# Performance work log

Hardware: AMD Instinct MI355X
Metric: run time of the kernel (lower is better)

The kernel has to match this reference:

```python
import jax, jax.numpy as jnp
import numpy as np

NUM_EXPERTS = 64
TOP_K = 2
AUX_COEF = 0.001
Z_COEF = 0.001


def setup_inputs() -> dict:
    key = jax.random.key(0)
    k1, k2 = jax.random.split(key)
    hidden_states = jax.random.normal(k1, (16384, 4096), dtype=jnp.float32)
    W_gate = jax.random.normal(k2, (NUM_EXPERTS, 4096), dtype=jnp.float32) * 0.02
    return {"hidden_states": hidden_states, "W_gate": W_gate}


def reference(hidden_states, W_gate):
    # Gate GEMM: [N, H] x [E, H]^T -> [N, E]
    router_logits = jnp.einsum('nh,eh->ne', hidden_states, W_gate)
    router_probs = jax.nn.softmax(router_logits, axis=-1)

    # Top-k selection + renormalization
    expert_weights, expert_indices = jax.lax.top_k(router_probs, TOP_K)
    expert_weights = expert_weights / jnp.sum(expert_weights, axis=-1, keepdims=True)

    # Load-balancing loss: num_experts * sum_i f_i * P_i
    num_tokens = router_probs.shape[0]
    one_hot = jax.nn.one_hot(expert_indices, NUM_EXPERTS, dtype=jnp.float32)  # [N, K, E]
    tokens_per_expert = one_hot.sum(axis=(0, 1))  # [E]
    f = tokens_per_expert / (num_tokens * TOP_K)
    P = router_probs.mean(axis=0)
    lb_loss = NUM_EXPERTS * jnp.sum(f * P)

    # Z-loss: mean of logsumexp(logits)^2
    log_z = jax.nn.logsumexp(router_logits, axis=-1)
    z_loss = jnp.mean(log_z ** 2)

    aux_loss = AUX_COEF * lb_loss + Z_COEF * z_loss
    return expert_weights, expert_indices, aux_loss
```

## Files before the change

kernel.cpp:

```cpp
#include <hip/hip_runtime.h>
#include <hip/hip_bf16.h>

#define NTOK 16384
#define HD   4096
#define NE   64
#define KSPLIT 4
#define KS    (HD / KSPLIT)
#define NSTEP (KS / 32)
#define SL2   68
#define W2OFF 256
#define W2JSTR 131072

typedef __bf16 bf16x8 __attribute__((ext_vector_type(8)));
typedef float  f32x4  __attribute__((ext_vector_type(4)));

__device__ __forceinline__ f32x4 mfma16(bf16x8 a, bf16x8 b, f32x4 c) {
    return __builtin_amdgcn_mfma_f32_16x16x32_bf16(a, b, c, 0, 0, 0);
}

__global__ void prep_kernel(const float* __restrict__ Wg, float* __restrict__ ws) {
    const int idx = blockIdx.x * 256 + threadIdx.x;
    if (blockIdx.x == 0 && threadIdx.x < 129) ws[threadIdx.x] = 0.0f;
    __bf16* W2 = (__bf16*)(ws + W2OFF);
    const float4* src = (const float4*)(Wg + (size_t)idx * 8);
    float4 q0 = src[0], q1 = src[1];
    float xs[8] = {q0.x, q0.y, q0.z, q0.w, q1.x, q1.y, q1.z, q1.w};
    bf16x8 hi, lo;
    #pragma unroll
    for (int e = 0; e < 8; ++e) {
        __bf16 h = (__bf16)xs[e];
        hi[e] = h;
        lo[e] = (__bf16)(xs[e] - (float)h);
    }
    *(bf16x8*)(W2 + (size_t)idx * 16)     = hi;
    *(bf16x8*)(W2 + (size_t)idx * 16 + 8) = lo;
}

__global__ __launch_bounds__(256, 4) void router_kernel(
    const float* __restrict__ hs,
    float* __restrict__ out,
    float* __restrict__ ws)
{
    __shared__ float sRed[4 * 16 * SL2];
    __shared__ float sInv[16];
    __shared__ float sPp[256];
    __shared__ float sCnt[64];
    __shared__ float sZ;

    const int tid  = threadIdx.x;
    const int t0   = blockIdx.x * 16;
    const int wv   = tid >> 6;
    const int lane = tid & 63;
    const int fm   = lane & 15;
    const int fq   = lane >> 4;

    if (tid < 64) sCnt[tid] = 0.0f;
    if (tid == 0) sZ = 0.0f;

    const __bf16* W2 = (const __bf16*)(ws + W2OFF);
    const int k0 = wv * KS;
    const float* aPtr = hs + (size_t)(t0 + fm) * HD + k0 + fq * 8;
    const int bOff = (fm * 512 + (k0 >> 3) + fq) * 16;

    f32x4 acc[4];
    #pragma unroll
    for (int j = 0; j < 4; ++j) acc[j] = (f32x4){0.f, 0.f, 0.f, 0.f};

    float4 a_raw[2][2];
    bf16x8 b_frag[2][4][2];

    a_raw[0][0] = *(const float4*)(aPtr);
    a_raw[0][1] = *(const float4*)(aPtr + 4);
    #pragma unroll
    for (int j = 0; j < 4; ++j) {
        const __bf16* bp = W2 + j * W2JSTR + bOff;
        b_frag[0][j][0] = *(const bf16x8*)(bp);
        b_frag[0][j][1] = *(const bf16x8*)(bp + 8);
    }

    #pragma unroll 2
    for (int it = 0; it < NSTEP; ++it) {
        const int cur = it & 1, nxt = cur ^ 1;
        if (it + 1 < NSTEP) {
            const float* ap = aPtr + (it + 1) * 32;
            a_raw[nxt][0] = *(const float4*)(ap);
            a_raw[nxt][1] = *(const float4*)(ap + 4);
            const __bf16* bp = W2 + bOff + (it + 1) * 64;
            #pragma unroll
            for (int j = 0; j < 4; ++j) {
                b_frag[nxt][j][0] = *(const bf16x8*)(bp + j * W2JSTR);
                b_frag[nxt][j][1] = *(const bf16x8*)(bp + j * W2JSTR + 8);
            }
        }
        float4 q0 = a_raw[cur][0], q1 = a_raw[cur][1];
        float xs[8] = {q0.x, q0.y, q0.z, q0.w, q1.x, q1.y, q1.z, q1.w};
        bf16x8 ahi, alo;
        #pragma unroll
        for (int e = 0; e < 8; ++e) {
            __bf16 h = (__bf16)xs[e];
            ahi[e] = h;
            alo[e] = (__bf16)(xs[e] - (float)h);
        }
        #pragma unroll
        for (int j = 0; j < 4; ++j) {
            acc[j] = mfma16(ahi, b_frag[cur][j][0], acc[j]);
            acc[j] = mfma16(alo, b_frag[cur][j][0], acc[j]);
            acc[j] = mfma16(ahi, b_frag[cur][j][1], acc[j]);
            acc[j] = mfma16(alo, b_frag[cur][j][1], acc[j]);
        }
    }

    {
        float* my = &sRed[wv * 16 * SL2];
        #pragma unroll
        for (int j = 0; j < 4; ++j)
            #pragma unroll
            for (int r = 0; r < 4; ++r)
                my[(fq * 4 + r) * SL2 + (j * 16 + fm)] = acc[j][r];
    }
    __syncthreads();
    for (int s = tid; s < 1024; s += 256) {
        const int t = s >> 6, e = s & 63;
        const int o = t * SL2 + e;
        sRed[o] = sRed[o] + sRed[16 * SL2 + o] + sRed[32 * SL2 + o] + sRed[48 * SL2 + o];
    }
    __syncthreads();

    const int g = tid >> 4;
    const int l = tid & 15;
    float* Lrow = &sRed[g * SL2 + l * 4];
    float lv[4];
    float m = -3.0e38f;
    #pragma unroll
    for (int c = 0; c < 4; ++c) { lv[c] = Lrow[c]; m = fmaxf(m, lv[c]); }
    m = fmaxf(m, __shfl_xor(m, 1, 64));
    m = fmaxf(m, __shfl_xor(m, 2, 64));
    m = fmaxf(m, __shfl_xor(m, 4, 64));
    m = fmaxf(m, __shfl_xor(m, 8, 64));

    float v1 = -3.0e38f, v2 = -3.0e38f; int i1 = 0, i2 = 0;
    float ssum = 0.0f;
    #pragma unroll
    for (int c = 0; c < 4; ++c) {
        const float val = lv[c]; const int idx = l * 4 + c;
        const float ev = __expf(val - m);
        Lrow[c] = ev;
        ssum += ev;
        if (val > v1) { v2 = v1; i2 = i1; v1 = val; i1 = idx; }
        else if (val > v2) { v2 = val; i2 = idx; }
    }
    ssum += __shfl_xor(ssum, 1, 64);
    ssum += __shfl_xor(ssum, 2, 64);
    ssum += __shfl_xor(ssum, 4, 64);
    ssum += __shfl_xor(ssum, 8, 64);

    #pragma unroll
    for (int s = 1; s <= 8; s <<= 1) {
        const float ov1 = __shfl_xor(v1, s, 64);
        const int   oi1 = __shfl_xor(i1, s, 64);
        const float ov2 = __shfl_xor(v2, s, 64);
        const int   oi2 = __shfl_xor(i2, s, 64);
        float n1, n2; int ni1, ni2;
        const bool ofirst = (ov1 > v1) || (ov1 == v1 && oi1 < i1);
        if (ofirst) {
            n1 = ov1; ni1 = oi1;
            const bool osec = (ov2 > v1) || (ov2 == v1 && oi2 < i1);
            n2 = osec ? ov2 : v1; ni2 = osec ? oi2 : i1;
        } else {
            n1 = v1; ni1 = i1;
            const bool asec = (v2 > ov1) || (v2 == ov1 && i2 < oi1);
            n2 = asec ? v2 : ov1; ni2 = asec ? i2 : oi1;
        }
        v1 = n1; i1 = ni1; v2 = n2; i2 = ni2;
    }

    if (l == 0) {
        const float e1 = __expf(v1 - m), e2 = __expf(v2 - m);
        const float winv = 1.0f / (e1 + e2);
        const int token = t0 + g;
        out[2 * token]     = e1 * winv;
        out[2 * token + 1] = e2 * winv;
        out[2 * NTOK + 2 * token]     = (float)i1;
        out[2 * NTOK + 2 * token + 1] = (float)i2;
        const float lse = m + __logf(ssum);
        atomicAdd(&sZ, lse * lse);
        atomicAdd(&sCnt[i1], 1.0f);
        atomicAdd(&sCnt[i2], 1.0f);
        sInv[g] = 1.0f / ssum;
    }
    __syncthreads();

    {
        const int e = tid & 63;
        const int q = tid >> 6;
        float part = 0.0f;
        #pragma unroll
        for (int t = 0; t < 4; ++t) {
            const int tok = q * 4 + t;
            part += sRed[tok * SL2 + e] * sInv[tok];
        }
        sPp[q * 64 + e] = part;
    }
    __syncthreads();
    if (tid < 64) {
        const float ps = sPp[tid] + sPp[64 + tid] + sPp[128 + tid] + sPp[192 + tid];
        atomicAdd(&ws[tid], ps);
        atomicAdd(&ws[64 + tid], sCnt[tid]);
    }
    if (tid == 0) atomicAdd(&ws[128], sZ);
}

__global__ void finalize_kernel(const float* __restrict__ ws, float* __restrict__ out) {
    const int e = threadIdx.x;
    const float P = ws[e] * (1.0f / NTOK);
    const float f = ws[64 + e] * (1.0f / (NTOK * 2));
    float term = f * P;
    #pragma unroll
    for (int s = 32; s >= 1; s >>= 1) term += __shfl_xor(term, s, 64);
    if (e == 0) {
        const float lb = 64.0f * term;
        const float z  = ws[128] * (1.0f / NTOK);
        out[4 * NTOK] = 0.001f * lb + 0.001f * z;
    }
}

extern "C" void kernel_launch(void* const* d_in, const int* in_sizes, int n_in,
                              void* d_out, int out_size, void* d_ws, size_t ws_size,
                              hipStream_t stream) {
    const float* hs = (const float*)d_in[0];
    const float* Wg = (const float*)d_in[1];
    float* out = (float*)d_out;
    float* ws  = (float*)d_ws;

    hipLaunchKernelGGL(prep_kernel, dim3(128), dim3(256), 0, stream, Wg, ws);
    hipLaunchKernelGGL(router_kernel, dim3(NTOK / 16), dim3(256), 0, stream, hs, out, ws);
    hipLaunchKernelGGL(finalize_kernel, dim3(1), dim3(64), 0, stream, ws, out);
}
```

Before: 430.8 us.

## Split router into K-split GEMM with LDS-staged weights and separate epilogue kernel

After: 542.4 us. 25.9% more time.

```diff
diff --git a/kernel.cpp b/kernel.cpp
--- a/kernel.cpp
+++ b/kernel.cpp
@@ -4,12 +4,14 @@
 #define NTOK 16384
 #define HD   4096
 #define NE   64
-#define KSPLIT 4
+#define KSPLIT 16
 #define KS    (HD / KSPLIT)
 #define NSTEP (KS / 32)
 #define SL2   68
-#define W2OFF 256
-#define W2JSTR 131072
+
+#define W2HI_OFF 256
+#define W2LO_OFF (W2HI_OFF + 131072)
+#define PART_OFF (W2LO_OFF + 131072)
 
 typedef __bf16 bf16x8 __attribute__((ext_vector_type(8)));
 typedef float  f32x4  __attribute__((ext_vector_type(4)));
@@ -21,123 +23,151 @@
 __global__ void prep_kernel(const float* __restrict__ Wg, float* __restrict__ ws) {
     const int idx = blockIdx.x * 256 + threadIdx.x;
     if (blockIdx.x == 0 && threadIdx.x < 129) ws[threadIdx.x] = 0.0f;
-    __bf16* W2 = (__bf16*)(ws + W2OFF);
-    const float4* src = (const float4*)(Wg + (size_t)idx * 8);
-    float4 q0 = src[0], q1 = src[1];
+    const int ln = idx & 63;
+    const int j  = (idx >> 6) & 3;
+    const int s  = (idx >> 8) & 7;
+    const int ks = idx >> 11;
+    const int e  = j * 16 + (ln & 15);
+    const int k  = ks * KS + s * 32 + (ln >> 4) * 8;
+    const float* src = Wg + (size_t)e * HD + k;
+    float4 q0 = *(const float4*)src;
+    float4 q1 = *(const float4*)(src + 4);
     float xs[8] = {q0.x, q0.y, q0.z, q0.w, q1.x, q1.y, q1.z, q1.w};
     bf16x8 hi, lo;
     #pragma unroll
-    for (int e = 0; e < 8; ++e) {
-        __bf16 h = (__bf16)xs[e];
-        hi[e] = h;
-        lo[e] = (__bf16)(xs[e] - (float)h);
-    }
-    *(bf16x8*)(W2 + (size_t)idx * 16)     = hi;
-    *(bf16x8*)(W2 + (size_t)idx * 16 + 8) = lo;
-}
-
-__global__ __launch_bounds__(256, 4) void router_kernel(
-    const float* __restrict__ hs,
-    float* __restrict__ out,
-    float* __restrict__ ws)
+    for (int t = 0; t < 8; ++t) {
+        __bf16 h = (__bf16)xs[t];
+        hi[t] = h;
+        lo[t] = (__bf16)(xs[t] - (float)h);
+    }
+    *((bf16x8*)((__bf16*)(ws + W2HI_OFF)) + idx) = hi;
+    *((bf16x8*)((__bf16*)(ws + W2LO_OFF)) + idx) = lo;
+}
+
+__global__ __launch_bounds__(512, 4) void gemm_kernel(
+    const float* __restrict__ hs, float* __restrict__ ws)
 {
-    __shared__ float sRed[4 * 16 * SL2];
+    __shared__ bf16x8 sBhi[2048];
+    __shared__ bf16x8 sBlo[2048];
+
+    const int tid = threadIdx.x;
+    const int ks  = blockIdx.x & 15;
+    const int tb  = blockIdx.x >> 4;
+
+    {
+        const bf16x8* ghi = (const bf16x8*)((const __bf16*)(ws + W2HI_OFF)) + ks * 2048;
+        const bf16x8* glo = (const bf16x8*)((const __bf16*)(ws + W2LO_OFF)) + ks * 2048;
+        #pragma unroll
+        for (int c = 0; c < 4; ++c) {
+            sBhi[c * 512 + tid] = ghi[c * 512 + tid];
+            sBlo[c * 512 + tid] = glo[c * 512 + tid];
+        }
+    }
+    __syncthreads();
+
+    const int wv   = tid >> 6;
+    const int lane = tid & 63;
+    const int fm   = lane & 15;
+    const int fq   = lane >> 4;
+    float* part = ws + PART_OFF + (size_t)ks * (NTOK * 64);
+
+    #pragma unroll 1
+    for (int g = 0; g < 4; ++g) {
+        const int tok0 = tb * 512 + wv * 64 + g * 16;
+        const float* aPtr = hs + (size_t)(tok0 + fm) * HD + ks * KS + fq * 8;
+
+        f32x4 acc[4];
+        #pragma unroll
+        for (int j = 0; j < 4; ++j) acc[j] = (f32x4){0.f, 0.f, 0.f, 0.f};
+
+        float4 aq[2][2];
+        aq[0][0] = *(const float4*)(aPtr);
+        aq[0][1] = *(const float4*)(aPtr + 4);
+        aq[1][0] = *(const float4*)(aPtr + 32);
+        aq[1][1] = *(const float4*)(aPtr + 36);
+        bf16x8 bh[2][4], bl[2][4];
+        #pragma unroll
+        for (int j = 0; j < 4; ++j) {
+            bh[0][j] = sBhi[j * 64 + lane];
+            bl[0][j] = sBlo[j * 64 + lane];
+        }
+
+        #pragma unroll
+        for (int s = 0; s < NSTEP; ++s) {
+            const int cur = s & 1, nxt = cur ^ 1;
+            float4 q0 = aq[cur][0], q1 = aq[cur][1];
+            if (s + 2 < NSTEP) {
+                aq[cur][0] = *(const float4*)(aPtr + (s + 2) * 32);
+                aq[cur][1] = *(const float4*)(aPtr + (s + 2) * 32 + 4);
+            }
+            if (s + 1 < NSTEP) {
+                #pragma unroll
+                for (int j = 0; j < 4; ++j) {
+                    bh[nxt][j] = sBhi[((s + 1) * 4 + j) * 64 + lane];
+                    bl[nxt][j] = sBlo[((s + 1) * 4 + j) * 64 + lane];
+                }
+            }
+            float xs[8] = {q0.x, q0.y, q0.z, q0.w, q1.x, q1.y, q1.z, q1.w};
+            bf16x8 ahi, alo;
+            #pragma unroll
+            for (int t = 0; t < 8; ++t) {
+                __bf16 h = (__bf16)xs[t];
+                ahi[t] = h;
+                alo[t] = (__bf16)(xs[t] - (float)h);
+            }
+            #pragma unroll
+            for (int j = 0; j < 4; ++j) {
+                acc[j] = mfma16(ahi, bh[cur][j], acc[j]);
+                acc[j] = mfma16(alo, bh[cur][j], acc[j]);
+                acc[j] = mfma16(ahi, bl[cur][j], acc[j]);
+                acc[j] = mfma16(alo, bl[cur][j], acc[j]);
+            }
+        }
+
+        #pragma unroll
+        for (int j = 0; j < 4; ++j)
+            #pragma unroll
+            for (int r = 0; r < 4; ++r)
+                part[(size_t)(tok0 + fq * 4 + r) * 64 + j * 16 + fm] = acc[j][r];
+    }
+}
+
+__global__ __launch_bounds__(256) void epilogue_kernel(
+    float* __restrict__ ws, float* __restrict__ out)
+{
+    __shared__ float sRed[16 * SL2];
     __shared__ float sInv[16];
     __shared__ float sPp[256];
     __shared__ float sCnt[64];
     __shared__ float sZ;
 
-    const int tid  = threadIdx.x;
-    const int t0   = blockIdx.x * 16;
-    const int wv   = tid >> 6;
-    const int lane = tid & 63;
-    const int fm   = lane & 15;
-    const int fq   = lane >> 4;
-
+    const int tid = threadIdx.x;
+    const int t0  = blockIdx.x * 16;
     if (tid < 64) sCnt[tid] = 0.0f;
     if (tid == 0) sZ = 0.0f;
 
-    const __bf16* W2 = (const __bf16*)(ws + W2OFF);
-    const int k0 = wv * KS;
-    const float* aPtr = hs + (size_t)(t0 + fm) * HD + k0 + fq * 8;
-    const int bOff = (fm * 512 + (k0 >> 3) + fq) * 16;
-
-    f32x4 acc[4];
-    #pragma unroll
-    for (int j = 0; j < 4; ++j) acc[j] = (f32x4){0.f, 0.f, 0.f, 0.f};
-
-    float4 a_raw[2][2];
-    bf16x8 b_frag[2][4][2];
-
-    a_raw[0][0] = *(const float4*)(aPtr);
-    a_raw[0][1] = *(const float4*)(aPtr + 4);
-    #pragma unroll
-    for (int j = 0; j < 4; ++j) {
-        const __bf16* bp = W2 + j * W2JSTR + bOff;
-        b_frag[0][j][0] = *(const bf16x8*)(bp);
-        b_frag[0][j][1] = *(const bf16x8*)(bp + 8);
-    }
-
-    #pragma unroll 2
-    for (int it = 0; it < NSTEP; ++it) {
-        const int cur = it & 1, nxt = cur ^ 1;
-        if (it + 1 < NSTEP) {
-            const float* ap = aPtr + (it + 1) * 32;
-            a_raw[nxt][0] = *(const float4*)(ap);
-            a_raw[nxt][1] = *(const float4*)(ap + 4);
-            const __bf16* bp = W2 + bOff + (it + 1) * 64;
-            #pragma unroll
-            for (int j = 0; j < 4; ++j) {
-                b_frag[nxt][j][0] = *(const bf16x8*)(bp + j * W2JSTR);
-                b_frag[nxt][j][1] = *(const bf16x8*)(bp + j * W2JSTR + 8);
-            }
-        }
-        float4 q0 = a_raw[cur][0], q1 = a_raw[cur][1];
-        float xs[8] = {q0.x, q0.y, q0.z, q0.w, q1.x, q1.y, q1.z, q1.w};
-        bf16x8 ahi, alo;
-        #pragma unroll
-        for (int e = 0; e < 8; ++e) {
-            __bf16 h = (__bf16)xs[e];
-            ahi[e] = h;
-            alo[e] = (__bf16)(xs[e] - (float)h);
-        }
-        #pragma unroll
-        for (int j = 0; j < 4; ++j) {
-            acc[j] = mfma16(ahi, b_frag[cur][j][0], acc[j]);
-            acc[j] = mfma16(alo, b_frag[cur][j][0], acc[j]);
-            acc[j] = mfma16(ahi, b_frag[cur][j][1], acc[j]);
-            acc[j] = mfma16(alo, b_frag[cur][j][1], acc[j]);
-        }
-    }
-
-    {
-        float* my = &sRed[wv * 16 * SL2];
-        #pragma unroll
-        for (int j = 0; j < 4; ++j)
-            #pragma unroll
-            for (int r = 0; r < 4; ++r)
-                my[(fq * 4 + r) * SL2 + (j * 16 + fm)] = acc[j][r];
-    }
-    __syncthreads();
-    for (int s = tid; s < 1024; s += 256) {
-        const int t = s >> 6, e = s & 63;
-        const int o = t * SL2 + e;
-        sRed[o] = sRed[o] + sRed[16 * SL2 + o] + sRed[32 * SL2 + o] + sRed[48 * SL2 + o];
-    }
-    __syncthreads();
-
     const int g = tid >> 4;
     const int l = tid & 15;
-    float* Lrow = &sRed[g * SL2 + l * 4];
-    float lv[4];
+    const int tok = t0 + g;
+    const float* pbase = ws + PART_OFF + (size_t)tok * 64 + l * 4;
+    float4 sv = {0.f, 0.f, 0.f, 0.f};
+    #pragma unroll
+    for (int k = 0; k < KSPLIT; ++k) {
+        float4 v = *(const float4*)(pbase + (size_t)k * (NTOK * 64));
+        sv.x += v.x; sv.y += v.y; sv.z += v.z; sv.w += v.w;
+    }
+    float lv[4] = {sv.x, sv.y, sv.z, sv.w};
+    __syncthreads();
+
     float m = -3.0e38f;
     #pragma unroll
-    for (int c = 0; c < 4; ++c) { lv[c] = Lrow[c]; m = fmaxf(m, lv[c]); }
+    for (int c = 0; c < 4; ++c) m = fmaxf(m, lv[c]);
     m = fmaxf(m, __shfl_xor(m, 1, 64));
     m = fmaxf(m, __shfl_xor(m, 2, 64));
     m = fmaxf(m, __shfl_xor(m, 4, 64));
     m = fmaxf(m, __shfl_xor(m, 8, 64));
 
+    float* Lrow = &sRed[g * SL2 + l * 4];
     float v1 = -3.0e38f, v2 = -3.0e38f; int i1 = 0, i2 = 0;
     float ssum = 0.0f;
     #pragma unroll
@@ -177,11 +207,10 @@
     if (l == 0) {
         const float e1 = __expf(v1 - m), e2 = __expf(v2 - m);
         const float winv = 1.0f / (e1 + e2);
-        const int token = t0 + g;
-        out[2 * token]     = e1 * winv;
-        out[2 * token + 1] = e2 * winv;
-        out[2 * NTOK + 2 * token]     = (float)i1;
-        out[2 * NTOK + 2 * token + 1] = (float)i2;
+        out[2 * tok]     = e1 * winv;
+        out[2 * tok + 1] = e2 * winv;
+        out[2 * NTOK + 2 * tok]     = (float)i1;
+        out[2 * NTOK + 2 * tok + 1] = (float)i2;
         const float lse = m + __logf(ssum);
         atomicAdd(&sZ, lse * lse);
         atomicAdd(&sCnt[i1], 1.0f);
@@ -193,13 +222,13 @@
     {
         const int e = tid & 63;
         const int q = tid >> 6;
-        float part = 0.0f;
+        float p = 0.0f;
         #pragma unroll
         for (int t = 0; t < 4; ++t) {
-            const int tok = q * 4 + t;
-            part += sRed[tok * SL2 + e] * sInv[tok];
-        }
-        sPp[q * 64 + e] = part;
+            const int tk = q * 4 + t;
+            p += sRed[tk * SL2 + e] * sInv[tk];
+        }
+        sPp[q * 64 + e] = p;
     }
     __syncthreads();
     if (tid < 64) {
@@ -233,6 +262,7 @@
     float* ws  = (float*)d_ws;
 
     hipLaunchKernelGGL(prep_kernel, dim3(128), dim3(256), 0, stream, Wg, ws);
-    hipLaunchKernelGGL(router_kernel, dim3(NTOK / 16), dim3(256), 0, stream, hs, out, ws);
+    hipLaunchKernelGGL(gemm_kernel, dim3(512), dim3(512), 0, stream, hs, ws);
+    hipLaunchKernelGGL(epilogue_kernel, dim3(NTOK / 16), dim3(256), 0, stream, ws, out);
     hipLaunchKernelGGL(finalize_kernel, dim3(1), dim3(64), 0, stream, ws, out);
 }
```

## Repack gate weights into fragment order and deepen load prefetch pipeline

Applied to the files above, without the earlier changes.

Measured after the change: 448.9 us. 4.2% more time.

```diff
diff --git a/kernel.cpp b/kernel.cpp
--- a/kernel.cpp
+++ b/kernel.cpp
@@ -4,12 +4,10 @@
 #define NTOK 16384
 #define HD   4096
 #define NE   64
-#define KSPLIT 4
-#define KS    (HD / KSPLIT)
-#define NSTEP (KS / 32)
-#define SL2   68
-#define W2OFF 256
-#define W2JSTR 131072
+#define SL2  68
+
+#define W2HI_OFF 256
+#define W2LO_OFF (W2HI_OFF + 131072)
 
 typedef __bf16 bf16x8 __attribute__((ext_vector_type(8)));
 typedef float  f32x4  __attribute__((ext_vector_type(4)));
@@ -21,22 +19,28 @@
 __global__ void prep_kernel(const float* __restrict__ Wg, float* __restrict__ ws) {
     const int idx = blockIdx.x * 256 + threadIdx.x;
     if (blockIdx.x == 0 && threadIdx.x < 129) ws[threadIdx.x] = 0.0f;
-    __bf16* W2 = (__bf16*)(ws + W2OFF);
-    const float4* src = (const float4*)(Wg + (size_t)idx * 8);
-    float4 q0 = src[0], q1 = src[1];
+    const int ln = idx & 63;
+    const int j  = (idx >> 6) & 3;
+    const int s  = (idx >> 8) & 7;
+    const int ks = idx >> 11;
+    const int e  = j * 16 + (ln & 15);
+    const int k  = ks * 256 + s * 32 + (ln >> 4) * 8;
+    const float* src = Wg + (size_t)e * HD + k;
+    float4 q0 = *(const float4*)src;
+    float4 q1 = *(const float4*)(src + 4);
     float xs[8] = {q0.x, q0.y, q0.z, q0.w, q1.x, q1.y, q1.z, q1.w};
     bf16x8 hi, lo;
     #pragma unroll
-    for (int e = 0; e < 8; ++e) {
-        __bf16 h = (__bf16)xs[e];
-        hi[e] = h;
-        lo[e] = (__bf16)(xs[e] - (float)h);
-    }
-    *(bf16x8*)(W2 + (size_t)idx * 16)     = hi;
-    *(bf16x8*)(W2 + (size_t)idx * 16 + 8) = lo;
-}
-
-__global__ __launch_bounds__(256, 4) void router_kernel(
+    for (int t = 0; t < 8; ++t) {
+        __bf16 h = (__bf16)xs[t];
+        hi[t] = h;
+        lo[t] = (__bf16)(xs[t] - (float)h);
+    }
+    *((bf16x8*)((__bf16*)(ws + W2HI_OFF)) + idx) = hi;
+    *((bf16x8*)((__bf16*)(ws + W2LO_OFF)) + idx) = lo;
+}
+
+__global__ __launch_bounds__(256, 3) void router_kernel(
     const float* __restrict__ hs,
     float* __restrict__ out,
     float* __restrict__ ws)
@@ -57,56 +61,61 @@
     if (tid < 64) sCnt[tid] = 0.0f;
     if (tid == 0) sZ = 0.0f;
 
-    const __bf16* W2 = (const __bf16*)(ws + W2OFF);
-    const int k0 = wv * KS;
-    const float* aPtr = hs + (size_t)(t0 + fm) * HD + k0 + fq * 8;
-    const int bOff = (fm * 512 + (k0 >> 3) + fq) * 16;
+    const bf16x8* Whi = (const bf16x8*)((const __bf16*)(ws + W2HI_OFF));
+    const bf16x8* Wlo = (const bf16x8*)((const __bf16*)(ws + W2LO_OFF));
+    const int cbase = wv * 8192 + lane;
+    const float* aPtr = hs + (size_t)(t0 + fm) * HD + wv * 1024 + fq * 8;
 
     f32x4 acc[4];
     #pragma unroll
     for (int j = 0; j < 4; ++j) acc[j] = (f32x4){0.f, 0.f, 0.f, 0.f};
 
-    float4 a_raw[2][2];
-    bf16x8 b_frag[2][4][2];
-
-    a_raw[0][0] = *(const float4*)(aPtr);
-    a_raw[0][1] = *(const float4*)(aPtr + 4);
-    #pragma unroll
-    for (int j = 0; j < 4; ++j) {
-        const __bf16* bp = W2 + j * W2JSTR + bOff;
-        b_frag[0][j][0] = *(const bf16x8*)(bp);
-        b_frag[0][j][1] = *(const bf16x8*)(bp + 8);
-    }
-
-    #pragma unroll 2
-    for (int it = 0; it < NSTEP; ++it) {
-        const int cur = it & 1, nxt = cur ^ 1;
-        if (it + 1 < NSTEP) {
-            const float* ap = aPtr + (it + 1) * 32;
-            a_raw[nxt][0] = *(const float4*)(ap);
-            a_raw[nxt][1] = *(const float4*)(ap + 4);
-            const __bf16* bp = W2 + bOff + (it + 1) * 64;
+    f32x4 aq[4][2];
+    #pragma unroll
+    for (int d = 0; d < 4; ++d) {
+        aq[d][0] = __builtin_nontemporal_load((const f32x4*)(aPtr + d * 32));
+        aq[d][1] = __builtin_nontemporal_load((const f32x4*)(aPtr + d * 32 + 4));
+    }
+    bf16x8 bh[2][4], bl[2][4];
+    #pragma unroll
+    for (int d = 0; d < 2; ++d)
+        #pragma unroll
+        for (int j = 0; j < 4; ++j) {
+            bh[d][j] = Whi[cbase + d * 256 + j * 64];
+            bl[d][j] = Wlo[cbase + d * 256 + j * 64];
+        }
+
+    #pragma unroll
+    for (int st = 0; st < 32; ++st) {
+        const int ab = st & 3, bb = st & 1;
+        f32x4 q0 = aq[ab][0], q1 = aq[ab][1];
+        float xs[8] = {q0.x, q0.y, q0.z, q0.w, q1.x, q1.y, q1.z, q1.w};
+        bf16x8 ahi, alo;
+        #pragma unroll
+        for (int t = 0; t < 8; ++t) {
+            __bf16 h = (__bf16)xs[t];
+            ahi[t] = h;
+            alo[t] = (__bf16)(xs[t] - (float)h);
+        }
+        {
+            const int nst = (st + 4 < 32) ? (st + 4) : 31;
+            aq[ab][0] = __builtin_nontemporal_load((const f32x4*)(aPtr + nst * 32));
+            aq[ab][1] = __builtin_nontemporal_load((const f32x4*)(aPtr + nst * 32 + 4));
+        }
+        #pragma unroll
+        for (int j = 0; j < 4; ++j) {
+            acc[j] = mfma16(ahi, bh[bb][j], acc[j]);
+            acc[j] = mfma16(alo, bh[bb][j], acc[j]);
+            acc[j] = mfma16(ahi, bl[bb][j], acc[j]);
+            acc[j] = mfma16(alo, bl[bb][j], acc[j]);
+        }
+        {
+            const int nst = (st + 2 < 32) ? (st + 2) : 31;
             #pragma unroll
             for (int j = 0; j < 4; ++j) {
-                b_frag[nxt][j][0] = *(const bf16x8*)(bp + j * W2JSTR);
-                b_frag[nxt][j][1] = *(const bf16x8*)(bp + j * W2JSTR + 8);
+                bh[bb][j] = Whi[cbase + nst * 256 + j * 64];
+                bl[bb][j] = Wlo[cbase + nst * 256 + j * 64];
             }
-        }
-        float4 q0 = a_raw[cur][0], q1 = a_raw[cur][1];
-        float xs[8] = {q0.x, q0.y, q0.z, q0.w, q1.x, q1.y, q1.z, q1.w};
-        bf16x8 ahi, alo;
-        #pragma unroll
-        for (int e = 0; e < 8; ++e) {
-            __bf16 h = (__bf16)xs[e];
-            ahi[e] = h;
-            alo[e] = (__bf16)(xs[e] - (float)h);
-        }
-        #pragma unroll
-        for (int j = 0; j < 4; ++j) {
-            acc[j] = mfma16(ahi, b_frag[cur][j][0], acc[j]);
-            acc[j] = mfma16(alo, b_frag[cur][j][0], acc[j]);
-            acc[j] = mfma16(ahi, b_frag[cur][j][1], acc[j]);
-            acc[j] = mfma16(alo, b_frag[cur][j][1], acc[j]);
         }
     }
 
@@ -193,13 +202,13 @@
     {
         const int e = tid & 63;
         const int q = tid >> 6;
-        float part = 0.0f;
+        float p = 0.0f;
         #pragma unroll
         for (int t = 0; t < 4; ++t) {
-            const int tok = q * 4 + t;
-            part += sRed[tok * SL2 + e] * sInv[tok];
-        }
-        sPp[q * 64 + e] = part;
+            const int tk = q * 4 + t;
+            p += sRed[tk * SL2 + e] * sInv[tk];
+        }
+        sPp[q * 64 + e] = p;
     }
     __syncthreads();
     if (tid < 64) {
```
